# Optimization experiments

Hardware: AMD Instinct MI355X
Metric: run time of the kernel (lower is better)

## Reference

```python
import jax, jax.numpy as jnp
import numpy as np

B, T, D, H, L = 64, 256, 1024, 1024, 4

def setup_inputs() -> dict:
    key = jax.random.key(0)
    k1, k2, k3 = jax.random.split(key, 3)
    x = jax.random.normal(k1, (B, T, D), dtype=jnp.float32)
    # Keras LSTMCell params per layer: kernel [D,4H], recurrent_kernel [H,4H], bias [4H]
    Ws = jax.random.normal(k2, (L, D, 4 * H), dtype=jnp.float32) * (1.0 / np.sqrt(D))
    Us = jax.random.normal(k3, (L, H, 4 * H), dtype=jnp.float32) * (1.0 / np.sqrt(H))
    # unit_forget_bias=True: forget-gate bias initialized to 1
    b = np.zeros((L, 4 * H), dtype=np.float32)
    b[:, H:2 * H] = 1.0
    return {"x": x, "Ws": Ws, "Us": Us, "bs": jnp.asarray(b)}

def _lstm_layer(x, W, U, b):
    # Precompute input projection for all timesteps: [B,T,4H]
    xz = jnp.einsum('btd,dg->btg', x, W) + b
    h0 = jnp.zeros((x.shape[0], U.shape[0]), x.dtype)
    c0 = jnp.zeros_like(h0)
    def step(carry, zt):
        h, c = carry
        z = zt + h @ U  # [B,4H]
        i, f, g, o = jnp.split(z, 4, axis=-1)
        i = jax.nn.sigmoid(i)
        f = jax.nn.sigmoid(f)
        g = jnp.tanh(g)
        o = jax.nn.sigmoid(o)
        c_new = f * c + i * g
        h_new = o * jnp.tanh(c_new)
        return (h_new, c_new), h_new
    _, hs = jax.lax.scan(step, (h0, c0), jnp.swapaxes(xz, 0, 1))  # hs: [T,B,H]
    return jnp.swapaxes(hs, 0, 1)  # [B,T,H]

def reference(x, Ws, Us, bs):
    seq = x
    for l in range(Ws.shape[0]):  # small fixed layer loop
        seq = _lstm_layer(seq, Ws[l], Us[l], bs[l])
    return seq
```

## Files before the change

### kernel.cpp

```cpp
#include <hip/hip_runtime.h>
#include <stdint.h>
#include <stddef.h>

typedef _Float16 f16;
typedef _Float16 f16x8 __attribute__((ext_vector_type(8)));
typedef float f32x4 __attribute__((ext_vector_type(4)));

#define MFMA16(a, b, c) __builtin_amdgcn_mfma_f32_16x16x32_f16((a), (b), (c), 0, 0, 0)

static constexpr int kB = 64;
static constexpr int kT = 256;
static constexpr int kD = 1024;
static constexpr int kH = 1024;
static constexpr int kG = 4096;
static constexpr int kSlot = 64 * 1024;
static constexpr int kNSlots = kT + 1;
static constexpr size_t kHistE = (size_t)kNSlots * kSlot;

__device__ __forceinline__ float fast_sigmoid(float x) {
  return __builtin_amdgcn_rcpf(1.f + __expf(-x));
}
__device__ __forceinline__ float fast_tanh(float x) {
  x = fminf(9.f, fmaxf(-9.f, x));
  const float e = __expf(2.f * x);
  return (e - 1.f) * __builtin_amdgcn_rcpf(e + 1.f);
}

__global__ void x_perm_cvt(const float* __restrict__ x, f16* __restrict__ xp) {
  const size_t id = (size_t)blockIdx.x * 256 + threadIdx.x;
  const int d8 = (int)(id & 127) << 3;
  const int b = (int)(id >> 7) & 63;
  const int t = (int)(id >> 13);
  const float* s = x + (((size_t)b * kT + t) << 10) + d8;
  float4 a = *(const float4*)(s);
  float4 c = *(const float4*)(s + 4);
  f16x8 o;
  o[0] = (f16)a.x; o[1] = (f16)a.y; o[2] = (f16)a.z; o[3] = (f16)a.w;
  o[4] = (f16)c.x; o[5] = (f16)c.y; o[6] = (f16)c.z; o[7] = (f16)c.w;
  *(f16x8*)(xp + (size_t)t * kSlot + (size_t)(d8 >> 3) * 512 + b * 8) = o;
}

__global__ void transpose_cvt_z(const float* __restrict__ src, f16* __restrict__ dst) {
  __shared__ float tile[32][33];
  const int z = blockIdx.z;
  const int c0 = blockIdx.x * 32;
  const int r0 = blockIdx.y * 32;
  const float* s = src + (size_t)z * kD * kG;
  f16* d = dst + (size_t)z * kG * kD;
  for (int rr = threadIdx.y; rr < 32; rr += 8)
    tile[rr][threadIdx.x] = s[(size_t)(r0 + rr) * kG + c0 + threadIdx.x];
  __syncthreads();
  for (int cc = threadIdx.y; cc < 32; cc += 8)
    d[(size_t)(c0 + cc) * kD + r0 + threadIdx.x] = (f16)tile[threadIdx.x][cc];
}

__launch_bounds__(1024, 1)
__global__ void lstm_scan2(const f16* __restrict__ below_lo,
                           const f16* __restrict__ Wt_lo, const f16* __restrict__ Ut_lo,
                           const f16* __restrict__ Wt_hi, const f16* __restrict__ Ut_hi,
                           f16* __restrict__ hist_lo, f16* __restrict__ hist_hi,
                           const float* __restrict__ bias_lo,
                           const float* __restrict__ bias_hi,
                           float* __restrict__ out32) {
  __shared__ f16 Cw[8192 * 8];
  __shared__ f16 red0h[2][12 * 64 * 4];
  __shared__ f16 red1h[2][12 * 64 * 4];
  __shared__ f16 hstage[4][16][8];

  const int bid = blockIdx.x;
  const int layerbit = bid & 1;
  const int wgl = bid >> 1;
  const int hbase = wgl * 8;
  const int tid = threadIdx.x;
  const int l = tid & 63, w = tid >> 6;
  const int lr = l & 15, lq = l >> 4;
  const int bw = w & 3, kw = w >> 2;

  const f16* Wt = layerbit ? Wt_hi : Wt_lo;
  const f16* Ut = layerbit ? Ut_hi : Ut_lo;
  f16* own_hist = layerbit ? hist_hi : hist_lo;
  const f16* below_base = layerbit ? (hist_lo + kSlot) : below_lo;
  const float* bias = layerbit ? bias_hi : bias_lo;

#pragma unroll
  for (int ff = 0; ff < 8; ++ff) {
    const int f = tid * 8 + ff;
    const int x = f >> 12, kkg = (f >> 6) & 63, fl = f & 63;
    const int flr = fl & 15, flq = fl >> 4;
    const int r = x * 16 + flr;
    const int grow = (r >> 3) * 1024 + hbase + (r & 7);
    const f16* src = (kkg < 32) ? Wt : Ut;
    *(f16x8*)&Cw[f * 8] =
        *(const f16x8*)(src + (size_t)grow * 1024 + (kkg & 31) * 32 + flq * 8);
  }

  float bv0 = 0.f, bv1 = 0.f;
  if (kw == 0) {
    bv0 = bias[((lr < 8) ? 0 : 1024) + hbase + (lr & 7)];
    bv1 = bias[((lr < 8) ? 2048 : 3072) + hbase + (lr & 7)];
  }
  __syncthreads();

  const int brow = bw * 16 + lq * 4;
  const int ugl = hbase + (lr & 7);
  const int row = bw * 16 + lr;
  const bool needs_poll = layerbit || (kw >= 2);

  float c_reg[4] = {0.f, 0.f, 0.f, 0.f};

#pragma unroll 1
  for (int t = 0; t < kT; ++t) {
    const f16* hsrc = (kw < 2) ? (below_base + (size_t)t * kSlot)
                               : (own_hist + (size_t)t * kSlot);
    const f16* hp = hsrc + (size_t)((kw & 1) * 64 + lq) * 512 + row * 8;

    f16x8 ha[16];
    if (needs_poll) {
      for (;;) {
#pragma unroll
        for (int ii = 0; ii < 16; ++ii)
          asm volatile("global_load_dwordx4 %0, %1, off sc0 sc1"
                       : "=v"(ha[ii]) : "v"(hp + (size_t)ii * 2048) : "memory");
        asm volatile("s_waitcnt vmcnt(0)" ::: "memory");
        __builtin_amdgcn_sched_barrier(0);
        bool ok = true;
#pragma unroll
        for (int ii = 0; ii < 16; ++ii) {
#pragma unroll
          for (int e = 0; e < 8; e += 2) {
            const f16 ev = ha[ii][e];
            const unsigned short bb = __builtin_bit_cast(unsigned short, ev);
            ok = ok && (bb != 0x7F7F);
          }
        }
        if (__all(ok)) break;
      }
    } else {
#pragma unroll
      for (int ii = 0; ii < 16; ++ii)
        ha[ii] = *(const f16x8*)(hp + (size_t)ii * 2048);
    }

    f32x4 acc0 = {}, acc1 = {};
    const int kkb = kw * 16;
#pragma unroll
    for (int ii = 0; ii < 16; ++ii) {
      const f16x8 b0 = *(const f16x8*)&Cw[((kkb + ii) * 64 + l) * 8];
      const f16x8 b1 = *(const f16x8*)&Cw[((4096 + (kkb + ii) * 64) + l) * 8];
      acc0 = MFMA16(ha[ii], b0, acc0);
      acc1 = MFMA16(ha[ii], b1, acc1);
    }

    if (kw != 0) {
      const int rb = ((w - 4) * 64 + l) * 4;
#pragma unroll
      for (int j = 0; j < 4; ++j) {
        red0h[t & 1][rb + j] = (f16)acc0[j];
        red1h[t & 1][rb + j] = (f16)acc1[j];
      }
    }
    __syncthreads();

    if (kw == 0) {
      f32x4 s0 = acc0, s1 = acc1;
#pragma unroll
      for (int q = 0; q < 3; ++q) {
        const int rb = ((q * 4 + bw) * 64 + l) * 4;
#pragma unroll
        for (int j = 0; j < 4; ++j) {
          s0[j] += (float)red0h[t & 1][rb + j];
          s1[j] += (float)red1h[t & 1][rb + j];
        }
      }

      float hv[4];
#pragma unroll
      for (int j = 0; j < 4; ++j) {
        const float z0 = s0[j] + bv0;
        const float z1 = s1[j] + bv1;
        const float q0 = __shfl_xor(z0, 8);
        const float q1 = __shfl_xor(z1, 8);
        const float zi = (lr & 8) ? q0 : z0;
        const float zf = (lr & 8) ? z0 : q0;
        const float zg = (lr & 8) ? q1 : z1;
        const float zo = (lr & 8) ? z1 : q1;
        const float iv = fast_sigmoid(zi);
        const float fv = fast_sigmoid(zf);
        const float gv = fast_tanh(zg);
        const float ov = fast_sigmoid(zo);
        const float cn = fv * c_reg[j] + iv * gv;
        c_reg[j] = cn;
        hv[j] = ov * fast_tanh(cn);
      }

      if (lr < 8) {
#pragma unroll
        for (int j = 0; j < 4; ++j)
          hstage[w][lq * 4 + j][lr] = (f16)hv[j];
      }
      if (l < 16) {
        const f16x8 hrow = *(const f16x8*)&hstage[w][l][0];
        f16* dst = own_hist + (size_t)(t + 1) * kSlot +
                   ((size_t)wgl * 64 + bw * 16 + l) * 8;
        asm volatile("global_store_dwordx4 %0, %1, off sc0 sc1"
                     :: "v"(dst), "v"(hrow) : "memory");
      }
      if (out32 && layerbit && lr < 8) {
#pragma unroll
        for (int j = 0; j < 4; ++j)
          out32[((size_t)(brow + j) * kT + t) * kH + ugl] = hv[j];
      }
    }
  }
}

extern "C" void kernel_launch(void* const* d_in, const int* in_sizes, int n_in,
                              void* d_out, int out_size, void* d_ws, size_t ws_size,
                              hipStream_t stream) {
  (void)in_sizes; (void)n_in; (void)out_size; (void)ws_size;
  const float* x = (const float*)d_in[0];
  const float* Ws = (const float*)d_in[1];
  const float* Us = (const float*)d_in[2];
  const float* bs = (const float*)d_in[3];
  char* ws = (char*)d_ws;

  const size_t kLayerW = (size_t)kG * kD * 2;
  const size_t kHistB = kHistE * 2;
  const size_t WT_OFF = 0;
  const size_t UT_OFF = WT_OFF + 4 * kLayerW;
  const size_t XP_OFF = UT_OFF + 4 * kLayerW;
  const size_t HH_OFF = XP_OFF + (size_t)kT * kSlot * 2;

  f16* Wt = (f16*)(ws + WT_OFF);
  f16* Ut = (f16*)(ws + UT_OFF);
  f16* xp = (f16*)(ws + XP_OFF);

  f16* hist[4];
  for (int i = 0; i < 4; ++i) hist[i] = (f16*)(ws + HH_OFF + i * kHistB);

  x_perm_cvt<<<8192, 256, 0, stream>>>(x, xp);
  transpose_cvt_z<<<dim3(kG / 32, kD / 32, 4), dim3(32, 8), 0, stream>>>(Ws, Wt);
  transpose_cvt_z<<<dim3(kG / 32, kD / 32, 4), dim3(32, 8), 0, stream>>>(Us, Ut);
  for (int i = 0; i < 4; ++i) {
    hipMemsetAsync(ws + HH_OFF + i * kHistB, 0, (size_t)kSlot * 2, stream);
    hipMemsetAsync(ws + HH_OFF + i * kHistB + (size_t)kSlot * 2, 0x7F,
                   (size_t)kT * kSlot * 2, stream);
  }

  lstm_scan2<<<256, 1024, 0, stream>>>(
      xp, Wt, Ut, Wt + (size_t)kG * kD, Ut + (size_t)kG * kD,
      hist[0], hist[1],
      bs, bs + kG, (float*)nullptr);
  lstm_scan2<<<256, 1024, 0, stream>>>(
      hist[1] + kSlot, Wt + 2 * (size_t)kG * kD, Ut + 2 * (size_t)kG * kD,
      Wt + 3 * (size_t)kG * kD, Ut + 3 * (size_t)kG * kD,
      hist[2], hist[3],
      bs + 2 * kG, bs + 3 * kG, (float*)d_out);
}
```

Before: 3.249 ms.

## Replace per-step block barrier with LDS token handshakes between producer and consumer waves

Removes the __syncthreads at every timestep. Producer waves (kw!=0) now publish a per-wave token in LDS after writing their partial sums, and consumer waves (kw==0) spin on the three tokens for their batch row. Consumers post a token once they have read the reduction buffer, which lets producers run up to two steps ahead on the double buffer. This decouples the waves so a wave stalled on polling global h does not hold up the others, at the cost of LDS spin loops and hand-placed memory ordering that may be fragile.

```diff
diff --git a/kernel.cpp b/kernel.cpp
--- a/kernel.cpp
+++ b/kernel.cpp
@@ -66,6 +66,8 @@
   __shared__ f16 red0h[2][12 * 64 * 4];
   __shared__ f16 red1h[2][12 * 64 * 4];
   __shared__ f16 hstage[4][16][8];
+  __shared__ int stTok[12];
+  __shared__ int consTok[4];
 
   const int bid = blockIdx.x;
   const int layerbit = bid & 1;
@@ -81,6 +83,9 @@
   f16* own_hist = layerbit ? hist_hi : hist_lo;
   const f16* below_base = layerbit ? (hist_lo + kSlot) : below_lo;
   const float* bias = layerbit ? bias_hi : bias_lo;
+
+  if (tid < 12) stTok[tid] = -1;
+  if (tid < 4) consTok[tid] = -1;
 
 #pragma unroll
   for (int ff = 0; ff < 8; ++ff) {
@@ -110,58 +115,107 @@
 
 #pragma unroll 1
   for (int t = 0; t < kT; ++t) {
-    const f16* hsrc = (kw < 2) ? (below_base + (size_t)t * kSlot)
-                               : (own_hist + (size_t)t * kSlot);
-    const f16* hp = hsrc + (size_t)((kw & 1) * 64 + lq) * 512 + row * 8;
-
-    f16x8 ha[16];
-    if (needs_poll) {
-      for (;;) {
+    if (kw != 0) {
+      {
+        volatile int* ct = &consTok[bw];
+        while (*ct < t - 2) {}
+        __asm__ __volatile__("" ::: "memory");
+      }
+      const f16* hsrc = (kw < 2) ? (below_base + (size_t)t * kSlot)
+                                 : (own_hist + (size_t)t * kSlot);
+      const f16* hp = hsrc + (size_t)((kw & 1) * 64 + lq) * 512 + row * 8;
+
+      f16x8 ha[16];
+      if (needs_poll) {
+        for (;;) {
+#pragma unroll
+          for (int ii = 0; ii < 16; ++ii)
+            asm volatile("global_load_dwordx4 %0, %1, off sc0 sc1"
+                         : "=v"(ha[ii]) : "v"(hp + (size_t)ii * 2048) : "memory");
+          asm volatile("s_waitcnt vmcnt(0)" ::: "memory");
+          __builtin_amdgcn_sched_barrier(0);
+          bool ok = true;
+#pragma unroll
+          for (int ii = 0; ii < 16; ++ii) {
+#pragma unroll
+            for (int e = 0; e < 8; e += 2) {
+              const f16 ev = ha[ii][e];
+              const unsigned short bb = __builtin_bit_cast(unsigned short, ev);
+              ok = ok && (bb != 0x7F7F);
+            }
+          }
+          if (__all(ok)) break;
+        }
+      } else {
 #pragma unroll
         for (int ii = 0; ii < 16; ++ii)
-          asm volatile("global_load_dwordx4 %0, %1, off sc0 sc1"
-                       : "=v"(ha[ii]) : "v"(hp + (size_t)ii * 2048) : "memory");
-        asm volatile("s_waitcnt vmcnt(0)" ::: "memory");
-        __builtin_amdgcn_sched_barrier(0);
-        bool ok = true;
-#pragma unroll
-        for (int ii = 0; ii < 16; ++ii) {
-#pragma unroll
-          for (int e = 0; e < 8; e += 2) {
-            const f16 ev = ha[ii][e];
-            const unsigned short bb = __builtin_bit_cast(unsigned short, ev);
-            ok = ok && (bb != 0x7F7F);
-          }
-        }
-        if (__all(ok)) break;
-      }
-    } else {
-#pragma unroll
-      for (int ii = 0; ii < 16; ++ii)
-        ha[ii] = *(const f16x8*)(hp + (size_t)ii * 2048);
-    }
-
-    f32x4 acc0 = {}, acc1 = {};
-    const int kkb = kw * 16;
-#pragma unroll
-    for (int ii = 0; ii < 16; ++ii) {
-      const f16x8 b0 = *(const f16x8*)&Cw[((kkb + ii) * 64 + l) * 8];
-      const f16x8 b1 = *(const f16x8*)&Cw[((4096 + (kkb + ii) * 64) + l) * 8];
-      acc0 = MFMA16(ha[ii], b0, acc0);
-      acc1 = MFMA16(ha[ii], b1, acc1);
-    }
-
-    if (kw != 0) {
+          ha[ii] = *(const f16x8*)(hp + (size_t)ii * 2048);
+      }
+
+      f32x4 acc0 = {}, acc1 = {};
+      const int kkb = kw * 16;
+#pragma unroll
+      for (int ii = 0; ii < 16; ++ii) {
+        const f16x8 b0 = *(const f16x8*)&Cw[((kkb + ii) * 64 + l) * 8];
+        const f16x8 b1 = *(const f16x8*)&Cw[((4096 + (kkb + ii) * 64) + l) * 8];
+        acc0 = MFMA16(ha[ii], b0, acc0);
+        acc1 = MFMA16(ha[ii], b1, acc1);
+      }
+
       const int rb = ((w - 4) * 64 + l) * 4;
 #pragma unroll
       for (int j = 0; j < 4; ++j) {
         red0h[t & 1][rb + j] = (f16)acc0[j];
         red1h[t & 1][rb + j] = (f16)acc1[j];
       }
-    }
-    __syncthreads();
-
-    if (kw == 0) {
+      asm volatile("s_waitcnt lgkmcnt(0)" ::: "memory");
+      __builtin_amdgcn_sched_barrier(0);
+      if (l == 0) *(volatile int*)&stTok[w - 4] = t;
+    } else {
+      const f16* hp = below_base + (size_t)t * kSlot + (size_t)lq * 512 + row * 8;
+      f16x8 ha[16];
+      if (needs_poll) {
+        for (;;) {
+#pragma unroll
+          for (int ii = 0; ii < 16; ++ii)
+            asm volatile("global_load_dwordx4 %0, %1, off sc0 sc1"
+                         : "=v"(ha[ii]) : "v"(hp + (size_t)ii * 2048) : "memory");
+          asm volatile("s_waitcnt vmcnt(0)" ::: "memory");
+          __builtin_amdgcn_sched_barrier(0);
+          bool ok = true;
+#pragma unroll
+          for (int ii = 0; ii < 16; ++ii) {
+#pragma unroll
+            for (int e = 0; e < 8; e += 2) {
+              const f16 ev = ha[ii][e];
+              const unsigned short bb = __builtin_bit_cast(unsigned short, ev);
+              ok = ok && (bb != 0x7F7F);
+            }
+          }
+          if (__all(ok)) break;
+        }
+      } else {
+#pragma unroll
+        for (int ii = 0; ii < 16; ++ii)
+          ha[ii] = *(const f16x8*)(hp + (size_t)ii * 2048);
+      }
+
+      f32x4 acc0 = {}, acc1 = {};
+#pragma unroll
+      for (int ii = 0; ii < 16; ++ii) {
+        const f16x8 b0 = *(const f16x8*)&Cw[(ii * 64 + l) * 8];
+        const f16x8 b1 = *(const f16x8*)&Cw[((4096 + ii * 64) + l) * 8];
+        acc0 = MFMA16(ha[ii], b0, acc0);
+        acc1 = MFMA16(ha[ii], b1, acc1);
+      }
+
+      {
+        volatile int* t0 = &stTok[bw];
+        volatile int* t1 = &stTok[4 + bw];
+        volatile int* t2 = &stTok[8 + bw];
+        while (*t0 < t || *t1 < t || *t2 < t) {}
+        __asm__ __volatile__("" ::: "memory");
+      }
       f32x4 s0 = acc0, s1 = acc1;
 #pragma unroll
       for (int q = 0; q < 3; ++q) {
@@ -172,6 +226,9 @@
           s1[j] += (float)red1h[t & 1][rb + j];
         }
       }
+      asm volatile("s_waitcnt lgkmcnt(0)" ::: "memory");
+      __builtin_amdgcn_sched_barrier(0);
+      if (l == 0) *(volatile int*)&consTok[bw] = t;
 
       float hv[4];
 #pragma unroll
@@ -196,10 +253,10 @@
       if (lr < 8) {
 #pragma unroll
         for (int j = 0; j < 4; ++j)
-          hstage[w][lq * 4 + j][lr] = (f16)hv[j];
+          hstage[bw][lq * 4 + j][lr] = (f16)hv[j];
       }
       if (l < 16) {
-        const f16x8 hrow = *(const f16x8*)&hstage[w][l][0];
+        const f16x8 hrow = *(const f16x8*)&hstage[bw][l][0];
         f16* dst = own_hist + (size_t)(t + 1) * kSlot +
                    ((size_t)wgl * 64 + bw * 16 + l) * 8;
         asm volatile("global_store_dwordx4 %0, %1, off sc0 sc1"
```

New measurement: 7.949 ms. 145% more time.
